# Kernel tuning notes

Hardware: AMD Instinct MI355X
Metric: run time of the kernel (lower is better)

## Reference

```python
import jax, jax.numpy as jnp
import numpy as np

T, K, D, CIN = 8, 64, 512, 1536  # timesteps, num_centers, redu_dim, input channels


def _conv(x, w, b=None, pad=0):
    y = jax.lax.conv_general_dilated(x, w, (1, 1), [(pad, pad), (pad, pad)],
                                     dimension_numbers=('NCHW', 'OIHW', 'NCHW'))
    return y if b is None else y + b[None, :, None, None]


def setup_inputs() -> dict:
    key = jax.random.key(0)
    ks = jax.random.split(key, 15)
    B, H, W = 32, 8, 8
    s = lambda i, shp: jax.random.normal(ks[i], shp, jnp.float32) * 0.05
    return dict(
        x=jax.random.normal(ks[0], (B * T, CIN, H, W), jnp.float32),
        redu_w=s(1, (D, CIN, 1, 1)), redu_b=s(2, (D,)),
        w_x=s(3, (K, D, 1, 1)),
        att_x=s(4, (K, K, 3, 3)), att_h_w=s(5, (K, K, 3, 3)), att_b=s(6, (K,)),
        share_w=s(7, (K, K, 3, 3)), share_b=s(8, (K,)),
        U_r=s(9, (K, K, 3, 3)), U_z=s(10, (K, K, 3, 3)), U_h=s(11, (K, K, 3, 3)),
        centers=s(12, (K, D)),
        fc1_w=s(13, (T * K // 16, T * K)), fc2_w=s(14, (T * K, T * K // 16)),
    )


def reference(x, redu_w, redu_b, w_x, att_x, att_h_w, att_b, share_w, share_b,
              U_r, U_z, U_h, centers, fc1_w, fc2_w):
    NT, _, H, W = x.shape
    B = NT // T
    xt = _conv(x, redu_w, redu_b)                    # (B*T, D, H, W) 1x1 reduction
    wxpb = _conv(xt, w_x)                            # (B*T, K, H, W)
    att_v = _conv(wxpb, att_x, pad=1).reshape(B, T, K, H, W).transpose(1, 0, 2, 3, 4)  # (T,B,K,H,W)
    wxpb5 = wxpb.reshape(B, T, K, H, W)

    def fc(v):  # ChannelAttention shared MLP (1x1 convs == matmuls)
        return jnp.maximum(v @ fc1_w.T, 0.) @ fc2_w.T

    def step(h, _):
        ah = _conv(h, att_h_w, att_b, pad=1)               # (B,K,H,W)
        e = jax.nn.relu(att_v + ah[None])                  # (T,B,K,H,W)
        e = e.transpose(1, 0, 2, 3, 4).reshape(B, T * K, H * W)
        g = jnp.tanh(fc(e.mean(-1)) + fc(e.max(-1)))       # (B, T*K) channel attention
        ex = jnp.exp(g.reshape(B, T, K))
        den = ex.sum(1, keepdims=True)
        den = den + (den == 0).astype(ex.dtype)
        alphas = ex / den                                  # softmax over timesteps
        wxt = (alphas[:, :, :, None, None] * wxpb5).sum(1) # (B,K,H,W)
        wxt = _conv(wxt, share_w, share_b, pad=1)
        z = jax.nn.sigmoid(wxt + _conv(h, U_z, pad=1))
        r = jax.nn.sigmoid(wxt + _conv(h, U_r, pad=1))
        hh = jnp.tanh(wxt + _conv(r * h, U_h, pad=1))
        h_new = (1. - z) * hh + z * h
        return h_new, h_new

    h0 = jnp.zeros((B, K, H, W), x.dtype)
    _, hs = jax.lax.scan(step, h0, None, length=T)         # (T,B,K,H,W)
    assigns = hs.transpose(1, 0, 2, 3, 4).reshape(B * T, K, H * W)
    a_sum = assigns.sum(-1, keepdims=True)                 # (B*T,K,1)
    a = a_sum * centers[None]                              # (B*T,K,D)
    feats = xt.reshape(B * T, D, H * W).transpose(0, 2, 1) # (B*T,HW,D)
    vlad = jnp.einsum('nks,nsd->nkd', assigns, feats) - a  # (B*T,K,D)
    vlad = vlad.reshape(B, T, K, D).sum(1)                 # (B,K,D)
    vlad = vlad / jnp.maximum(jnp.linalg.norm(vlad, axis=2, keepdims=True), 1e-12)
    vlad = vlad.reshape(B, K * D)
    vlad = vlad / jnp.maximum(jnp.linalg.norm(vlad, axis=1, keepdims=True), 1e-12)
    return vlad
```

## Files before the change

kernel.cpp:

```cpp
#include <hip/hip_runtime.h>
#include <math.h>

#define T_   8
#define K_   64
#define D_   512
#define CIN_ 1536
#define B_   32
#define S_   64
#define NT_  256

#define WLO_BF16  786432u
#define WXT_OFF   786432u
#define XT_OFF    819200u
#define WXPB_OFF  9207808u
#define ATTV_OFF  10256384u
#define HS_OFF    11436032u
#define ASUM_OFF  13041664u
#define WPB       25034752u
#define WATTX_BF16 20512768u

typedef __bf16 v8bf __attribute__((ext_vector_type(8)));
typedef __bf16 v4bf __attribute__((ext_vector_type(4)));
typedef float  v4f  __attribute__((ext_vector_type(4)));
typedef _Float16 v4h __attribute__((ext_vector_type(4)));
typedef _Float16 v8h __attribute__((ext_vector_type(8)));

__global__ __launch_bounds__(256) void k_prep(const float* __restrict__ redu_w,
                                              const float* __restrict__ w_x,
                                              float* __restrict__ ws) {
    unsigned idx = blockIdx.x * 256u + threadIdx.x;
    if (idx < 786432u) {
        float f = redu_w[idx];
        __bf16 h = (__bf16)f;
        __bf16 l = (__bf16)(f - (float)h);
        __bf16* wb = (__bf16*)ws;
        wb[idx] = h;
        wb[WLO_BF16 + idx] = l;
    } else if (idx < 819200u) {
        unsigned i = idx - 786432u;
        unsigned dd = i >> 6, k = i & 63u;
        ws[WXT_OFF + i] = w_x[k * 512u + dd];
    }
}

__global__ __launch_bounds__(256) void k_prep_w(const float* __restrict__ w0,
                                                const float* __restrict__ w1,
                                                const float* __restrict__ w2,
                                                const float* __restrict__ w3,
                                                const float* __restrict__ w4,
                                                const float* __restrict__ w5,
                                                float* __restrict__ ws) {
    unsigned idx = blockIdx.x * 256u + threadIdx.x;
    if (idx >= 221184u) return;
    unsigned w = idx / 36864u, r = idx % 36864u;
    const float* src = (w == 0) ? w0 : (w == 1) ? w1 : (w == 2) ? w2
                     : (w == 3) ? w3 : (w == 4) ? w4 : w5;
    float f = src[r];
    __bf16 h = (__bf16)f;
    __bf16 l = (__bf16)(f - (float)h);
    unsigned o = r / 576u, rem = r % 576u, ii = rem / 9u, dydx = rem % 9u;
    __bf16* wb = (__bf16*)ws;
    if (w < 5u) {
        unsigned dst = WPB + w * 73728u + (dydx * 64u + o) * 64u + ii;
        wb[dst] = h;
        wb[dst + 36864u] = l;
    } else {
        wb[WATTX_BF16 + (dydx * 64u + o) * 64u + ii] = h;
    }
}

__global__ __launch_bounds__(256) void k_gemm_xt_mfma(const float* __restrict__ x,
                                                      const float* __restrict__ redu_b,
                                                      float* __restrict__ ws) {
    __shared__ __bf16 xhi_s[64 * 72];
    __shared__ __bf16 xlo_s[64 * 72];
    const __bf16* __restrict__ Whi = (const __bf16*)ws;
    const __bf16* __restrict__ Wlo = ((const __bf16*)ws) + WLO_BF16;
    float* xt = ws + XT_OFF;
    const int n = blockIdx.y;
    const int d0 = blockIdx.x * 256;
    const int tid = threadIdx.x;
    const int wave = tid >> 6, lane = tid & 63;
    const int lrow = lane & 15, lkg = lane >> 4;
    const int m_base = d0 + wave * 64;
    const float* __restrict__ xn = x + n * 98304;
    const int s4 = tid & 15, cb = tid >> 4;

    v4f acc[4][4];
#pragma unroll
    for (int mt = 0; mt < 4; ++mt)
#pragma unroll
        for (int nt = 0; nt < 4; ++nt) acc[mt][nt] = (v4f){0.f, 0.f, 0.f, 0.f};

    for (int c0 = 0; c0 < 1536; c0 += 64) {
        float4 v[4];
#pragma unroll
        for (int j = 0; j < 4; ++j)
            v[j] = *(const float4*)&xn[(c0 + cb * 4 + j) * 64 + s4 * 4];
        __syncthreads();
#pragma unroll
        for (int i = 0; i < 4; ++i) {
            v4bf hv, lv;
#pragma unroll
            for (int j = 0; j < 4; ++j) {
                float f = ((const float*)&v[j])[i];
                __bf16 h = (__bf16)f;
                hv[j] = h;
                lv[j] = (__bf16)(f - (float)h);
            }
            int row = s4 * 4 + i;
            *(v4bf*)&xhi_s[row * 72 + cb * 4] = hv;
            *(v4bf*)&xlo_s[row * 72 + cb * 4] = lv;
        }
        __syncthreads();
#pragma unroll
        for (int ks = 0; ks < 64; ks += 32) {
            v8bf bh[4], bl[4], ah[4], al[4];
#pragma unroll
            for (int nt = 0; nt < 4; ++nt) {
                int off = (nt * 16 + lrow) * 72 + ks + lkg * 8;
                bh[nt] = *(const v8bf*)&xhi_s[off];
                bl[nt] = *(const v8bf*)&xlo_s[off];
            }
#pragma unroll
            for (int mt = 0; mt < 4; ++mt) {
                int gi = (m_base + mt * 16 + lrow) * 1536 + c0 + ks + lkg * 8;
                ah[mt] = *(const v8bf*)&Whi[gi];
                al[mt] = *(const v8bf*)&Wlo[gi];
            }
#pragma unroll
            for (int mt = 0; mt < 4; ++mt)
#pragma unroll
                for (int nt = 0; nt < 4; ++nt) {
                    acc[mt][nt] = __builtin_amdgcn_mfma_f32_16x16x32_bf16(
                        ah[mt], bh[nt], acc[mt][nt], 0, 0, 0);
                    acc[mt][nt] = __builtin_amdgcn_mfma_f32_16x16x32_bf16(
                        ah[mt], bl[nt], acc[mt][nt], 0, 0, 0);
                    acc[mt][nt] = __builtin_amdgcn_mfma_f32_16x16x32_bf16(
                        al[mt], bh[nt], acc[mt][nt], 0, 0, 0);
                }
        }
    }
#pragma unroll
    for (int mt = 0; mt < 4; ++mt) {
#pragma unroll
        for (int r = 0; r < 4; ++r) {
            int m = m_base + mt * 16 + lkg * 4 + r;
            float bias = redu_b[m];
#pragma unroll
            for (int nt = 0; nt < 4; ++nt) {
                int s = nt * 16 + lrow;
                xt[(n * 512 + m) * 64 + s] = acc[mt][nt][r] + bias;
            }
        }
    }
}

__global__ __launch_bounds__(256) void k_gemm_wxpb(float* __restrict__ ws) {
    __shared__ float Aw[16 * 64];
    __shared__ float Bx[16 * 64];
    const float* wxT = ws + WXT_OFF;
    const float* xt = ws + XT_OFF;
    float* wxpb = ws + WXPB_OFF;
    const int n = blockIdx.x;
    const int tid = threadIdx.x;
    const int sg = tid & 15, kg = tid >> 4;

    float acc[4][4];
#pragma unroll
    for (int i = 0; i < 4; ++i)
#pragma unroll
        for (int j = 0; j < 4; ++j) acc[i][j] = 0.f;

    for (int d0 = 0; d0 < 512; d0 += 16) {
        int cc = tid >> 4, q = tid & 15;
        *(float4*)&Aw[cc * 64 + q * 4] = *(const float4*)&wxT[(d0 + cc) * 64 + q * 4];
        *(float4*)&Bx[cc * 64 + q * 4] = *(const float4*)&xt[n * 32768 + (d0 + cc) * 64 + q * 4];
        __syncthreads();
#pragma unroll
        for (int c2 = 0; c2 < 16; ++c2) {
            float4 a = *(const float4*)&Aw[c2 * 64 + kg * 4];
            float4 b = *(const float4*)&Bx[c2 * 64 + sg * 4];
            float av[4] = {a.x, a.y, a.z, a.w};
            float bv[4] = {b.x, b.y, b.z, b.w};
#pragma unroll
            for (int i = 0; i < 4; ++i)
#pragma unroll
                for (int j = 0; j < 4; ++j)
                    acc[i][j] = fmaf(av[i], bv[j], acc[i][j]);
        }
        __syncthreads();
    }
#pragma unroll
    for (int i = 0; i < 4; ++i) {
        float4 o = {acc[i][0], acc[i][1], acc[i][2], acc[i][3]};
        *(float4*)&wxpb[(n * 64 + kg * 4 + i) * 64 + sg * 4] = o;
    }
}

__device__ __forceinline__ void conv_mfma(const __bf16* __restrict__ Wh,
                                          const __bf16* tS,
                                          int l15, int kg8, int mt, v4f acc[4]) {
    v8bf vz;
#pragma unroll
    for (int q = 0; q < 8; ++q) vz[q] = (__bf16)0.f;
#pragma unroll
    for (int i = 0; i < 4; ++i) acc[i] = (v4f){0.f, 0.f, 0.f, 0.f};
    const int yb = l15 >> 3, xb = l15 & 7;
    v8bf wh[9][2];
#pragma unroll
    for (int p = 0; p < 9; ++p) {
        const int wrow = (p * 64 + mt * 16 + l15) * 64 + kg8;
#pragma unroll
        for (int kci = 0; kci < 2; ++kci)
            wh[p][kci] = *(const v8bf*)&Wh[wrow + kci * 32];
    }
#pragma unroll
    for (int dy = 0; dy < 3; ++dy)
#pragma unroll
        for (int dx = 0; dx < 3; ++dx) {
            const int x0 = xb + dx - 1;
            const bool okx = (unsigned)x0 < 8u;
#pragma unroll
            for (int i = 0; i < 4; ++i) {
                const int y0 = yb + dy - 1 + 2 * i;
                const bool ok = ((unsigned)y0 < 8u) & okx;
                const int s0 = ((y0 * 8 + x0) & 63) * 72 + kg8;
#pragma unroll
                for (int kci = 0; kci < 2; ++kci) {
                    v8bf b = ok ? *(const v8bf*)&tS[s0 + kci * 32] : vz;
                    acc[i] = __builtin_amdgcn_mfma_f32_16x16x32_bf16(
                        wh[dy * 3 + dx][kci], b, acc[i], 0, 0, 0);
                }
            }
        }
}

__device__ __forceinline__ void conv_mfma3(const __bf16* __restrict__ W0,
                                           const __bf16* __restrict__ W1,
                                           const __bf16* __restrict__ W2,
                                           const __bf16* tS,
                                           int l15, int kg8, int mt,
                                           v4f a0[4], v4f a1[4], v4f a2[4]) {
    v8bf vz;
#pragma unroll
    for (int q = 0; q < 8; ++q) vz[q] = (__bf16)0.f;
#pragma unroll
    for (int i = 0; i < 4; ++i) {
        a0[i] = (v4f){0.f, 0.f, 0.f, 0.f};
        a1[i] = (v4f){0.f, 0.f, 0.f, 0.f};
        a2[i] = (v4f){0.f, 0.f, 0.f, 0.f};
    }
    const int yb = l15 >> 3, xb = l15 & 7;
#pragma unroll
    for (int dy = 0; dy < 3; ++dy) {
        v8bf w0[3][2], w1[3][2], w2[3][2];
#pragma unroll
        for (int dx = 0; dx < 3; ++dx) {
            const int wrow = ((dy * 3 + dx) * 64 + mt * 16 + l15) * 64 + kg8;
#pragma unroll
            for (int kci = 0; kci < 2; ++kci) {
                w0[dx][kci] = *(const v8bf*)&W0[wrow + kci * 32];
                w1[dx][kci] = *(const v8bf*)&W1[wrow + kci * 32];
                w2[dx][kci] = *(const v8bf*)&W2[wrow + kci * 32];
            }
        }
#pragma unroll
        for (int dx = 0; dx < 3; ++dx) {
            const int x0 = xb + dx - 1;
            const bool okx = (unsigned)x0 < 8u;
#pragma unroll
            for (int i = 0; i < 4; ++i) {
                const int y0 = yb + dy - 1 + 2 * i;
                const bool ok = ((unsigned)y0 < 8u) & okx;
                const int s0 = ((y0 * 8 + x0) & 63) * 72 + kg8;
#pragma unroll
                for (int kci = 0; kci < 2; ++kci) {
                    v8bf b = ok ? *(const v8bf*)&tS[s0 + kci * 32] : vz;
                    a0[i] = __builtin_amdgcn_mfma_f32_16x16x32_bf16(w0[dx][kci], b, a0[i], 0, 0, 0);
                    a1[i] = __builtin_amdgcn_mfma_f32_16x16x32_bf16(w1[dx][kci], b, a1[i], 0, 0, 0);
                    a2[i] = __builtin_amdgcn_mfma_f32_16x16x32_bf16(w2[dx][kci], b, a2[i], 0, 0, 0);
                }
            }
        }
    }
}

__global__ __launch_bounds__(256) void k_recur(const float* __restrict__ att_b,
                                               const float* __restrict__ share_b,
                                               const float* __restrict__ fc1_w,
                                               const float* __restrict__ fc2_w,
                                               float* __restrict__ ws) {
    __shared__ float h_s[4096];
    __shared__ __attribute__((aligned(16))) __bf16 tA[64 * 72];
    __shared__ float cA[64 * 65];
    __shared__ float cB[64 * 65];
    __shared__ float misc[1088];
    __shared__ __attribute__((aligned(16))) _Float16 attv_s[32768];
    const int b = blockIdx.x, tid = threadIdx.x;
    const int lane = tid & 63;
    const int wave = tid >> 6;
    const int mt = wave;
    const int l15 = lane & 15, kg = lane >> 4, kg8 = kg * 8;
    const __bf16* Wp = (const __bf16*)ws + WPB;
    const __bf16* Wattx = (const __bf16*)ws + WATTX_BF16;
    const float* wxpb = ws + WXPB_OFF;
    float* hsg = ws + HS_OFF;
    float* asg = ws + ASUM_OFF;

    for (int i = tid; i < 4096; i += 256) h_s[i] = 0.f;

    for (int tp = 0; tp < 8; ++tp) {
        const float* src = wxpb + (b * 8 + tp) * 4096;
        for (int i = tid; i < 4096; i += 256) {
            int k = i >> 6, s = i & 63;
            tA[s * 72 + k] = (__bf16)src[i];
        }
        __syncthreads();
        v4f av[4];
        conv_mfma(Wattx, tA, l15, kg8, mt, av);
#pragma unroll
        for (int i2 = 0; i2 < 4; ++i2)
#pragma unroll
            for (int r = 0; r < 4; ++r)
                attv_s[tp * 4096 + (mt * 16 + kg * 4 + r) * 64 + i2 * 16 + l15] =
                    (_Float16)av[i2][r];
        __syncthreads();
    }

    float abvr[2];
#pragma unroll
    for (int rep = 0; rep < 2; ++rep) abvr[rep] = att_b[(tid + rep * 256) >> 3];
    float sb4[4];
#pragma unroll
    for (int r = 0; r < 4; ++r) sb4[r] = share_b[mt * 16 + kg * 4 + r];

    for (int t = 0; t < 8; ++t) {
#pragma unroll
        for (int rep = 0; rep < 2; ++rep) {
            int s = tid & 63, g = (tid >> 6) + rep * 4;
#pragma unroll
            for (int q4 = 0; q4 < 2; ++q4) {
                v4bf hv;
#pragma unroll
                for (int q = 0; q < 4; ++q) hv[q] = (__bf16)h_s[(g * 8 + q4 * 4 + q) * 64 + s];
                *(v4bf*)&tA[s * 72 + g * 8 + q4 * 4] = hv;
            }
        }
        __syncthreads();
        v4f az[4], ar[4];
        {
            v4f a[4];
            conv_mfma3(Wp, Wp + 2u * 73728u, Wp + 3u * 73728u, tA,
                       l15, kg8, mt, a, az, ar);
#pragma unroll
            for (int i = 0; i < 4; ++i)
#pragma unroll
                for (int r = 0; r < 4; ++r)
                    cA[(mt * 16 + kg * 4 + r) * 65 + i * 16 + l15] = a[i][r];
        }
        __syncthreads();
#pragma unroll
        for (int rep = 0; rep < 2; ++rep) {
            int vt = tid + rep * 256;
            int kk = vt >> 3, yy = vt & 7;
            float ah8[8];
            const float* cr = &cA[kk * 65 + yy * 8];
#pragma unroll
            for (int xx = 0; xx < 8; ++xx) ah8[xx] = cr[xx] + abvr[rep];
            for (int tp = 0; tp < 8; ++tp) {
                v8h va = *(const v8h*)&attv_s[tp * 4096 + kk * 64 + yy * 8];
                float s_ = 0.f, m_ = 0.f;
#pragma unroll
                for (int xx = 0; xx < 8; ++xx) {
                    float v = fmaxf((float)va[xx] + ah8[xx], 0.f);
                    s_ += v;
                    m_ = fmaxf(m_, v);
                }
                s_ += __shfl_down(s_, 4, 8);
                s_ += __shfl_down(s_, 2, 8);
                s_ += __shfl_down(s_, 1, 8);
                m_ = fmaxf(m_, __shfl_down(m_, 4, 8));
                m_ = fmaxf(m_, __shfl_down(m_, 2, 8));
                m_ = fmaxf(m_, __shfl_down(m_, 1, 8));
                if (yy == 0) {
                    misc[tp * 64 + kk] = s_ * (1.f / 64.f);
                    misc[512 + tp * 64 + kk] = m_;
                }
            }
        }
        __syncthreads();
        {
            int i2 = tid >> 2, part = tid & 3;
            int i = i2 & 31;
            const float* src = misc + ((i2 < 32) ? 0 : 512);
            const float* wrow = fc1_w + i * 512 + part * 128;
            const float* s2 = src + part * 128;
            float pa[4] = {0.f, 0.f, 0.f, 0.f};
#pragma unroll
            for (int c4 = 0; c4 < 32; ++c4) {
                float4 wv = *(const float4*)&wrow[c4 * 4];
                float4 sv = *(const float4*)&s2[c4 * 4];
                float* pp = &pa[c4 & 3];
                *pp = fmaf(wv.x, sv.x, *pp);
                *pp = fmaf(wv.y, sv.y, *pp);
                *pp = fmaf(wv.z, sv.z, *pp);
                *pp = fmaf(wv.w, sv.w, *pp);
            }
            float p = (pa[0] + pa[1]) + (pa[2] + pa[3]);
            p += __shfl_down(p, 2, 4);
            p += __shfl_down(p, 1, 4);
            if (part == 0) misc[1024 + i2] = fmaxf(p, 0.f);
        }
        __syncthreads();
#pragma unroll
        for (int rep = 0; rep < 2; ++rep) {
            int vt = tid + rep * 256;
            const float* w2 = fc2_w + vt * 32;
            float gm = 0.f, gx = 0.f;
#pragma unroll
            for (int i4 = 0; i4 < 8; ++i4) {
                float4 wv = *(const float4*)&w2[i4 * 4];
                gm = fmaf(wv.x, misc[1024 + i4 * 4 + 0], gm);
                gm = fmaf(wv.y, misc[1024 + i4 * 4 + 1], gm);
                gm = fmaf(wv.z, misc[1024 + i4 * 4 + 2], gm);
                gm = fmaf(wv.w, misc[1024 + i4 * 4 + 3], gm);
                gx = fmaf(wv.x, misc[1056 + i4 * 4 + 0], gx);
                gx = fmaf(wv.y, misc[1056 + i4 * 4 + 1], gx);
                gx = fmaf(wv.z, misc[1056 + i4 * 4 + 2], gx);
                gx = fmaf(wv.w, misc[1056 + i4 * 4 + 3], gx);
            }
            misc[vt] = expf(tanhf(gm + gx));
        }
        __syncthreads();
#pragma unroll
        for (int rep = 0; rep < 2; ++rep) {
            int vt = tid + rep * 256;
            int k6 = vt & 63;
            float den = 0.f;
#pragma unroll
            for (int tp = 0; tp < 8; ++tp) den += misc[tp * 64 + k6];
            den += (den == 0.f) ? 1.f : 0.f;
            misc[512 + vt] = misc[vt] / den;
        }
        __syncthreads();
#pragma unroll
        for (int rep = 0; rep < 2; ++rep) {
            int vt = tid + rep * 256;
            int kk = vt >> 3, yy = vt & 7;
            float wx8[8];
#pragma unroll
            for (int xx = 0; xx < 8; ++xx) wx8[xx] = 0.f;
            const float* src0 = wxpb + b * 32768 + kk * 64 + yy * 8;
#pragma unroll
            for (int tp = 0; tp < 8; ++tp) {
                float al = misc[512 + tp * 64 + kk];
                float4 v0 = *(const float4*)&src0[tp * 4096];
                float4 v1 = *(const float4*)&src0[tp * 4096 + 4];
                float v[8] = {v0.x, v0.y, v0.z, v0.w, v1.x, v1.y, v1.z, v1.w};
#pragma unroll
                for (int xx = 0; xx < 8; ++xx) wx8[xx] = fmaf(al, v[xx], wx8[xx]);
            }
#pragma unroll
            for (int xx = 0; xx < 8; ++xx) tA[(yy * 8 + xx) * 72 + kk] = (__bf16)wx8[xx];
        }
        __syncthreads();
        v4f ash[4];
        conv_mfma(Wp + 1u * 73728u, tA, l15, kg8, mt, ash);
        float zf[4][4], wof[4][4];
#pragma unroll
        for (int i = 0; i < 4; ++i)
#pragma unroll
            for (int r = 0; r < 4; ++r) {
                int ko = mt * 16 + kg * 4 + r;
                int s = i * 16 + l15;
                float wo = ash[i][r] + sb4[r];
                float z = 1.f / (1.f + expf(-(wo + az[i][r])));
                float rr = 1.f / (1.f + expf(-(wo + ar[i][r])));
                cB[ko * 65 + s] = rr * h_s[ko * 64 + s];
                zf[i][r] = z;
                wof[i][r] = wo;
            }
        __syncthreads();
#pragma unroll
        for (int rep = 0; rep < 2; ++rep) {
            int s = tid & 63, g = (tid >> 6) + rep * 4;
#pragma unroll
            for (int q4 = 0; q4 < 2; ++q4) {
                v4bf hv;
#pragma unroll
                for (int q = 0; q < 4; ++q) hv[q] = (__bf16)cB[(g * 8 + q4 * 4 + q) * 65 + s];
                *(v4bf*)&tA[s * 72 + g * 8 + q4 * 4] = hv;
            }
        }
        __syncthreads();
        {
            v4f ach[4];
            conv_mfma(Wp + 4u * 73728u, tA, l15, kg8, mt, ach);
#pragma unroll
            for (int r = 0; r < 4; ++r) {
                int ko = mt * 16 + kg * 4 + r;
                float rsum = 0.f;
#pragma unroll
                for (int i = 0; i < 4; ++i) {
                    int s = i * 16 + l15;
                    float hh = tanhf(wof[i][r] + ach[i][r]);
                    float hold = h_s[ko * 64 + s];
                    float hn = (1.f - zf[i][r]) * hh + zf[i][r] * hold;
                    h_s[ko * 64 + s] = hn;
                    hsg[((t * 32 + b) * 64 + ko) * 64 + s] = hn;
                    rsum += hn;
                }
                rsum += __shfl_xor(rsum, 8, 16);
                rsum += __shfl_xor(rsum, 4, 16);
                rsum += __shfl_xor(rsum, 2, 16);
                rsum += __shfl_xor(rsum, 1, 16);
                if (l15 == 0) misc[1024 + ko] = rsum;
            }
        }
        __syncthreads();
        if (tid < 64) asg[b * 512 + t * 64 + tid] = misc[1024 + tid];
        __syncthreads();
    }
}

__global__ __launch_bounds__(256) void k_vlad(const float* __restrict__ centers,
                                              const float* __restrict__ ws,
                                              float* __restrict__ out) {
    __shared__ float As[16 * 68];
    __shared__ float Bs[16 * 68];
    const int b = blockIdx.y;
    const int d0 = blockIdx.x * 64;
    const int tid = threadIdx.x;
    const int kq = tid & 15, dq = tid >> 4;
    const int lk = tid >> 2, q = tid & 3;
    const float* hs = ws + HS_OFF;
    const float* xt = ws + XT_OFF;
    float acc[4][4];
#pragma unroll
    for (int i = 0; i < 4; ++i)
#pragma unroll
        for (int j = 0; j < 4; ++j) acc[i][j] = 0.f;

    for (int rc = 0; rc < 512; rc += 16) {
        int t = rc >> 6, hw0 = rc & 63;
        float4 va = *(const float4*)&hs[((t * 32 + b) * 64 + lk) * 64 + hw0 + q * 4];
        float4 vb = *(const float4*)&xt[(b * 8 + t) * 32768 + (d0 + lk) * 64 + hw0 + q * 4];
        __syncthreads();
        As[(q * 4 + 0) * 68 + lk] = va.x;
        As[(q * 4 + 1) * 68 + lk] = va.y;
        As[(q * 4 + 2) * 68 + lk] = va.z;
        As[(q * 4 + 3) * 68 + lk] = va.w;
        Bs[(q * 4 + 0) * 68 + lk] = vb.x;
        Bs[(q * 4 + 1) * 68 + lk] = vb.y;
        Bs[(q * 4 + 2) * 68 + lk] = vb.z;
        Bs[(q * 4 + 3) * 68 + lk] = vb.w;
        __syncthreads();
#pragma unroll
        for (int cc = 0; cc < 16; ++cc) {
            float4 a = *(const float4*)&As[cc * 68 + kq * 4];
            float4 bb = *(const float4*)&Bs[cc * 68 + dq * 4];
            float av[4] = {a.x, a.y, a.z, a.w};
            float bv[4] = {bb.x, bb.y, bb.z, bb.w};
#pragma unroll
            for (int i = 0; i < 4; ++i)
#pragma unroll
                for (int j = 0; j < 4; ++j)
                    acc[i][j] = fmaf(av[i], bv[j], acc[i][j]);
        }
    }
    const float* asum = ws + ASUM_OFF;
#pragma unroll
    for (int i = 0; i < 4; ++i) {
        int k = kq * 4 + i;
        float at = 0.f;
#pragma unroll
        for (int tp = 0; tp < 8; ++tp) at += asum[b * 512 + tp * 64 + k];
        float4 cen = *(const float4*)&centers[k * 512 + d0 + dq * 4];
        float4 o = {acc[i][0] - at * cen.x, acc[i][1] - at * cen.y,
                    acc[i][2] - at * cen.z, acc[i][3] - at * cen.w};
        *(float4*)&out[b * 32768 + k * 512 + d0 + dq * 4] = o;
    }
}

__global__ __launch_bounds__(64) void k_norm1(float* __restrict__ out) {
    const int b = blockIdx.x >> 6, k = blockIdx.x & 63;
    float* p = out + b * 32768 + k * 512;
    const int tid = threadIdx.x;
    float v[8];
    float ss = 0.f;
#pragma unroll
    for (int i = 0; i < 8; ++i) {
        v[i] = p[tid + i * 64];
        ss = fmaf(v[i], v[i], ss);
    }
#pragma unroll
    for (int off = 32; off > 0; off >>= 1) ss += __shfl_down(ss, off, 64);
    ss = __shfl(ss, 0, 64);
    float sc = 1.f / fmaxf(sqrtf(ss), 1e-12f);
#pragma unroll
    for (int i = 0; i < 8; ++i) p[tid + i * 64] = v[i] * sc;
}

__global__ __launch_bounds__(256) void k_norm2(float* __restrict__ out) {
    __shared__ float red[4];
    __shared__ float stot;
    const int b = blockIdx.x;
    const int tid = threadIdx.x;
    float* p = out + b * 32768;
    float ss = 0.f;
    for (int i = 0; i < 32; ++i) {
        float4 v = *(const float4*)&p[tid * 4 + i * 1024];
        ss += v.x * v.x + v.y * v.y + v.z * v.z + v.w * v.w;
    }
#pragma unroll
    for (int off = 32; off > 0; off >>= 1) ss += __shfl_down(ss, off, 64);
    if ((tid & 63) == 0) red[tid >> 6] = ss;
    __syncthreads();
    if (tid == 0) stot = 1.f / fmaxf(sqrtf(red[0] + red[1] + red[2] + red[3]), 1e-12f);
    __syncthreads();
    float sc = stot;
    for (int i = 0; i < 32; ++i) {
        float4 v = *(const float4*)&p[tid * 4 + i * 1024];
        v.x *= sc; v.y *= sc; v.z *= sc; v.w *= sc;
        *(float4*)&p[tid * 4 + i * 1024] = v;
    }
}

extern "C" void kernel_launch(void* const* d_in, const int* in_sizes, int n_in,
                              void* d_out, int out_size, void* d_ws, size_t ws_size,
                              hipStream_t stream) {
    const float* x       = (const float*)d_in[0];
    const float* redu_w  = (const float*)d_in[1];
    const float* redu_b  = (const float*)d_in[2];
    const float* w_x     = (const float*)d_in[3];
    const float* att_x   = (const float*)d_in[4];
    const float* att_h_w = (const float*)d_in[5];
    const float* att_b   = (const float*)d_in[6];
    const float* share_w = (const float*)d_in[7];
    const float* share_b = (const float*)d_in[8];
    const float* U_r     = (const float*)d_in[9];
    const float* U_z     = (const float*)d_in[10];
    const float* U_h     = (const float*)d_in[11];
    const float* centers = (const float*)d_in[12];
    const float* fc1_w   = (const float*)d_in[13];
    const float* fc2_w   = (const float*)d_in[14];
    float* ws = (float*)d_ws;
    float* out = (float*)d_out;

    k_prep<<<dim3(3200), dim3(256), 0, stream>>>(redu_w, w_x, ws);
    k_prep_w<<<dim3(864), dim3(256), 0, stream>>>(att_h_w, share_w, U_z, U_r, U_h,
                                                  att_x, ws);
    k_gemm_xt_mfma<<<dim3(2, 256), dim3(256), 0, stream>>>(x, redu_b, ws);
    k_gemm_wxpb<<<dim3(256), dim3(256), 0, stream>>>(ws);
    k_recur<<<dim3(32), dim3(256), 0, stream>>>(att_b, share_b, fc1_w, fc2_w, ws);
    k_vlad<<<dim3(8, 32), dim3(256), 0, stream>>>(centers, ws, out);
    k_norm1<<<dim3(2048), dim3(64), 0, stream>>>(out);
    k_norm2<<<dim3(32), dim3(256), 0, stream>>>(out);
}
```

Baseline: 697.8 us.

## Compose reduction and w_x weights, overlap xt GEMM with recurrence

Precomputes the combined weight W2 = w_x·redu_w, plus its folded bias, so wxpb is computed straight from x with one MFMA GEMM and no longer waits for xt. The full xt GEMM is moved into extra blocks of the recurrence kernel, so it runs alongside the 32 recurrence blocks and fills otherwise idle CUs. This removes the serial xt→wxpb dependency. The cost is an extra weight-composition kernel and some shift in rounding from the split-bf16 composed weights.

```diff
diff --git a/kernel.cpp b/kernel.cpp
--- a/kernel.cpp
+++ b/kernel.cpp
@@ -18,6 +18,9 @@
 #define ASUM_OFF  13041664u
 #define WPB       25034752u
 #define WATTX_BF16 20512768u
+#define W2HI_BF16  20549632u
+#define W2LO_BF16  20647936u
+#define B2_OFF     11435968u
 
 typedef __bf16 v8bf __attribute__((ext_vector_type(8)));
 typedef __bf16 v4bf __attribute__((ext_vector_type(4)));
@@ -26,7 +29,6 @@
 typedef _Float16 v8h __attribute__((ext_vector_type(8)));
 
 __global__ __launch_bounds__(256) void k_prep(const float* __restrict__ redu_w,
-                                              const float* __restrict__ w_x,
                                               float* __restrict__ ws) {
     unsigned idx = blockIdx.x * 256u + threadIdx.x;
     if (idx < 786432u) {
@@ -36,10 +38,6 @@
         __bf16* wb = (__bf16*)ws;
         wb[idx] = h;
         wb[WLO_BF16 + idx] = l;
-    } else if (idx < 819200u) {
-        unsigned i = idx - 786432u;
-        unsigned dd = i >> 6, k = i & 63u;
-        ws[WXT_OFF + i] = w_x[k * 512u + dd];
     }
 }
 
@@ -69,28 +67,60 @@
     }
 }
 
-__global__ __launch_bounds__(256) void k_gemm_xt_mfma(const float* __restrict__ x,
-                                                      const float* __restrict__ redu_b,
-                                                      float* __restrict__ ws) {
+__global__ __launch_bounds__(256) void k_w2(const float* __restrict__ w_x,
+                                            const float* __restrict__ redu_w,
+                                            const float* __restrict__ redu_b,
+                                            float* __restrict__ ws) {
+    __shared__ float wrow[512];
+    __shared__ float red[256];
+    const int k = blockIdx.x;
+    const int tid = threadIdx.x;
+    wrow[tid] = w_x[k * 512 + tid];
+    wrow[tid + 256] = w_x[k * 512 + tid + 256];
+    __syncthreads();
+    float acc[6] = {0.f, 0.f, 0.f, 0.f, 0.f, 0.f};
+    for (int d = 0; d < 512; ++d) {
+        float w = wrow[d];
+        const float* rr = &redu_w[d * 1536 + tid];
+#pragma unroll
+        for (int j = 0; j < 6; ++j) acc[j] = fmaf(w, rr[j * 256], acc[j]);
+    }
+    __bf16* wb = (__bf16*)ws;
+#pragma unroll
+    for (int j = 0; j < 6; ++j) {
+        int c = tid + j * 256;
+        __bf16 h = (__bf16)acc[j];
+        __bf16 l = (__bf16)(acc[j] - (float)h);
+        wb[W2HI_BF16 + k * 1536 + c] = h;
+        wb[W2LO_BF16 + k * 1536 + c] = l;
+    }
+    float p = wrow[tid] * redu_b[tid] + wrow[tid + 256] * redu_b[tid + 256];
+    red[tid] = p;
+    __syncthreads();
+    for (int off = 128; off > 0; off >>= 1) {
+        if (tid < off) red[tid] += red[tid + off];
+        __syncthreads();
+    }
+    if (tid == 0) ws[B2_OFF + k] = red[0];
+}
+
+__global__ __launch_bounds__(256) void k_wxpb_direct(const float* __restrict__ x,
+                                                     float* __restrict__ ws) {
     __shared__ __bf16 xhi_s[64 * 72];
     __shared__ __bf16 xlo_s[64 * 72];
-    const __bf16* __restrict__ Whi = (const __bf16*)ws;
-    const __bf16* __restrict__ Wlo = ((const __bf16*)ws) + WLO_BF16;
-    float* xt = ws + XT_OFF;
-    const int n = blockIdx.y;
-    const int d0 = blockIdx.x * 256;
+    const __bf16* __restrict__ W2h = (const __bf16*)ws + W2HI_BF16;
+    const __bf16* __restrict__ W2l = (const __bf16*)ws + W2LO_BF16;
+    float* wxpb = ws + WXPB_OFF;
+    const int n = blockIdx.x;
     const int tid = threadIdx.x;
     const int wave = tid >> 6, lane = tid & 63;
     const int lrow = lane & 15, lkg = lane >> 4;
-    const int m_base = d0 + wave * 64;
     const float* __restrict__ xn = x + n * 98304;
     const int s4 = tid & 15, cb = tid >> 4;
 
-    v4f acc[4][4];
-#pragma unroll
-    for (int mt = 0; mt < 4; ++mt)
-#pragma unroll
-        for (int nt = 0; nt < 4; ++nt) acc[mt][nt] = (v4f){0.f, 0.f, 0.f, 0.f};
+    v4f acc[4];
+#pragma unroll
+    for (int nt = 0; nt < 4; ++nt) acc[nt] = (v4f){0.f, 0.f, 0.f, 0.f};
 
     for (int c0 = 0; c0 < 1536; c0 += 64) {
         float4 v[4];
@@ -115,86 +145,31 @@
         __syncthreads();
 #pragma unroll
         for (int ks = 0; ks < 64; ks += 32) {
-            v8bf bh[4], bl[4], ah[4], al[4];
+            v8bf bh[4], bl[4];
 #pragma unroll
             for (int nt = 0; nt < 4; ++nt) {
                 int off = (nt * 16 + lrow) * 72 + ks + lkg * 8;
                 bh[nt] = *(const v8bf*)&xhi_s[off];
                 bl[nt] = *(const v8bf*)&xlo_s[off];
             }
-#pragma unroll
-            for (int mt = 0; mt < 4; ++mt) {
-                int gi = (m_base + mt * 16 + lrow) * 1536 + c0 + ks + lkg * 8;
-                ah[mt] = *(const v8bf*)&Whi[gi];
-                al[mt] = *(const v8bf*)&Wlo[gi];
-            }
-#pragma unroll
-            for (int mt = 0; mt < 4; ++mt)
-#pragma unroll
-                for (int nt = 0; nt < 4; ++nt) {
-                    acc[mt][nt] = __builtin_amdgcn_mfma_f32_16x16x32_bf16(
-                        ah[mt], bh[nt], acc[mt][nt], 0, 0, 0);
-                    acc[mt][nt] = __builtin_amdgcn_mfma_f32_16x16x32_bf16(
-                        ah[mt], bl[nt], acc[mt][nt], 0, 0, 0);
-                    acc[mt][nt] = __builtin_amdgcn_mfma_f32_16x16x32_bf16(
-                        al[mt], bh[nt], acc[mt][nt], 0, 0, 0);
-                }
-        }
-    }
-#pragma unroll
-    for (int mt = 0; mt < 4; ++mt) {
-#pragma unroll
-        for (int r = 0; r < 4; ++r) {
-            int m = m_base + mt * 16 + lkg * 4 + r;
-            float bias = redu_b[m];
+            int gi = (wave * 16 + lrow) * 1536 + c0 + ks + lkg * 8;
+            v8bf ah = *(const v8bf*)&W2h[gi];
+            v8bf al = *(const v8bf*)&W2l[gi];
 #pragma unroll
             for (int nt = 0; nt < 4; ++nt) {
-                int s = nt * 16 + lrow;
-                xt[(n * 512 + m) * 64 + s] = acc[mt][nt][r] + bias;
-            }
-        }
-    }
-}
-
-__global__ __launch_bounds__(256) void k_gemm_wxpb(float* __restrict__ ws) {
-    __shared__ float Aw[16 * 64];
-    __shared__ float Bx[16 * 64];
-    const float* wxT = ws + WXT_OFF;
-    const float* xt = ws + XT_OFF;
-    float* wxpb = ws + WXPB_OFF;
-    const int n = blockIdx.x;
-    const int tid = threadIdx.x;
-    const int sg = tid & 15, kg = tid >> 4;
-
-    float acc[4][4];
-#pragma unroll
-    for (int i = 0; i < 4; ++i)
-#pragma unroll
-        for (int j = 0; j < 4; ++j) acc[i][j] = 0.f;
-
-    for (int d0 = 0; d0 < 512; d0 += 16) {
-        int cc = tid >> 4, q = tid & 15;
-        *(float4*)&Aw[cc * 64 + q * 4] = *(const float4*)&wxT[(d0 + cc) * 64 + q * 4];
-        *(float4*)&Bx[cc * 64 + q * 4] = *(const float4*)&xt[n * 32768 + (d0 + cc) * 64 + q * 4];
-        __syncthreads();
-#pragma unroll
-        for (int c2 = 0; c2 < 16; ++c2) {
-            float4 a = *(const float4*)&Aw[c2 * 64 + kg * 4];
-            float4 b = *(const float4*)&Bx[c2 * 64 + sg * 4];
-            float av[4] = {a.x, a.y, a.z, a.w};
-            float bv[4] = {b.x, b.y, b.z, b.w};
-#pragma unroll
-            for (int i = 0; i < 4; ++i)
-#pragma unroll
-                for (int j = 0; j < 4; ++j)
-                    acc[i][j] = fmaf(av[i], bv[j], acc[i][j]);
-        }
-        __syncthreads();
-    }
-#pragma unroll
-    for (int i = 0; i < 4; ++i) {
-        float4 o = {acc[i][0], acc[i][1], acc[i][2], acc[i][3]};
-        *(float4*)&wxpb[(n * 64 + kg * 4 + i) * 64 + sg * 4] = o;
+                acc[nt] = __builtin_amdgcn_mfma_f32_16x16x32_bf16(ah, bh[nt], acc[nt], 0, 0, 0);
+                acc[nt] = __builtin_amdgcn_mfma_f32_16x16x32_bf16(ah, bl[nt], acc[nt], 0, 0, 0);
+                acc[nt] = __builtin_amdgcn_mfma_f32_16x16x32_bf16(al, bh[nt], acc[nt], 0, 0, 0);
+            }
+        }
+    }
+#pragma unroll
+    for (int r = 0; r < 4; ++r) {
+        int m = wave * 16 + lkg * 4 + r;
+        float bias = ws[B2_OFF + m];
+#pragma unroll
+        for (int nt = 0; nt < 4; ++nt)
+            wxpb[(n * 64 + m) * 64 + nt * 16 + lrow] = acc[nt][r] + bias;
     }
 }
 
@@ -286,10 +261,12 @@
     }
 }
 
-__global__ __launch_bounds__(256) void k_recur(const float* __restrict__ att_b,
+__global__ __launch_bounds__(256) void k_fused(const float* __restrict__ att_b,
                                                const float* __restrict__ share_b,
                                                const float* __restrict__ fc1_w,
                                                const float* __restrict__ fc2_w,
+                                               const float* __restrict__ x,
+                                               const float* __restrict__ redu_b,
                                                float* __restrict__ ws) {
     __shared__ float h_s[4096];
     __shared__ __attribute__((aligned(16))) __bf16 tA[64 * 72];
@@ -297,7 +274,95 @@
     __shared__ float cB[64 * 65];
     __shared__ float misc[1088];
     __shared__ __attribute__((aligned(16))) _Float16 attv_s[32768];
-    const int b = blockIdx.x, tid = threadIdx.x;
+    const int tid = threadIdx.x;
+
+    if (blockIdx.x >= 32) {
+        const int gb = blockIdx.x - 32;
+        const int n = gb >> 1;
+        const int d0 = (gb & 1) * 256;
+        const __bf16* __restrict__ Whi = (const __bf16*)ws;
+        const __bf16* __restrict__ Wlo = ((const __bf16*)ws) + WLO_BF16;
+        float* xt = ws + XT_OFF;
+        const int wave = tid >> 6, lane = tid & 63;
+        const int lrow = lane & 15, lkg = lane >> 4;
+        const int m_base = d0 + wave * 64;
+        const float* __restrict__ xn = x + n * 98304;
+        const int s4 = tid & 15, cb = tid >> 4;
+        __bf16* gxhi = (__bf16*)attv_s;
+        __bf16* gxlo = gxhi + 4608;
+
+        v4f acc[4][4];
+#pragma unroll
+        for (int mt = 0; mt < 4; ++mt)
+#pragma unroll
+            for (int nt = 0; nt < 4; ++nt) acc[mt][nt] = (v4f){0.f, 0.f, 0.f, 0.f};
+
+        for (int c0 = 0; c0 < 1536; c0 += 64) {
+            float4 v[4];
+#pragma unroll
+            for (int j = 0; j < 4; ++j)
+                v[j] = *(const float4*)&xn[(c0 + cb * 4 + j) * 64 + s4 * 4];
+            __syncthreads();
+#pragma unroll
+            for (int i = 0; i < 4; ++i) {
+                v4bf hv, lv;
+#pragma unroll
+                for (int j = 0; j < 4; ++j) {
+                    float f = ((const float*)&v[j])[i];
+                    __bf16 h = (__bf16)f;
+                    hv[j] = h;
+                    lv[j] = (__bf16)(f - (float)h);
+                }
+                int row = s4 * 4 + i;
+                *(v4bf*)&gxhi[row * 72 + cb * 4] = hv;
+                *(v4bf*)&gxlo[row * 72 + cb * 4] = lv;
+            }
+            __syncthreads();
+#pragma unroll
+            for (int ks = 0; ks < 64; ks += 32) {
+                v8bf bh[4], bl[4], ah[4], al[4];
+#pragma unroll
+                for (int nt = 0; nt < 4; ++nt) {
+                    int off = (nt * 16 + lrow) * 72 + ks + lkg * 8;
+                    bh[nt] = *(const v8bf*)&gxhi[off];
+                    bl[nt] = *(const v8bf*)&gxlo[off];
+                }
+#pragma unroll
+                for (int mt = 0; mt < 4; ++mt) {
+                    int gi = (m_base + mt * 16 + lrow) * 1536 + c0 + ks + lkg * 8;
+                    ah[mt] = *(const v8bf*)&Whi[gi];
+                    al[mt] = *(const v8bf*)&Wlo[gi];
+                }
+#pragma unroll
+                for (int mt = 0; mt < 4; ++mt)
+#pragma unroll
+                    for (int nt = 0; nt < 4; ++nt) {
+                        acc[mt][nt] = __builtin_amdgcn_mfma_f32_16x16x32_bf16(
+                            ah[mt], bh[nt], acc[mt][nt], 0, 0, 0);
+                        acc[mt][nt] = __builtin_amdgcn_mfma_f32_16x16x32_bf16(
+                            ah[mt], bl[nt], acc[mt][nt], 0, 0, 0);
+                        acc[mt][nt] = __builtin_amdgcn_mfma_f32_16x16x32_bf16(
+                            al[mt], bh[nt], acc[mt][nt], 0, 0, 0);
+                    }
+            }
+        }
+#pragma unroll
+        for (int mt = 0; mt < 4; ++mt) {
+#pragma unroll
+            for (int r = 0; r < 4; ++r) {
+                int m = m_base + mt * 16 + lkg * 4 + r;
+                float bias = redu_b[m];
+#pragma unroll
+                for (int nt = 0; nt < 4; ++nt) {
+                    int s = nt * 16 + lrow;
+                    xt[(n * 512 + m) * 64 + s] = acc[mt][nt][r] + bias;
+                }
+            }
+        }
+        return;
+    }
+
+    const int b = blockIdx.x;
     const int lane = tid & 63;
     const int wave = tid >> 6;
     const int mt = wave;
@@ -648,12 +713,13 @@
     float* ws = (float*)d_ws;
     float* out = (float*)d_out;
 
-    k_prep<<<dim3(3200), dim3(256), 0, stream>>>(redu_w, w_x, ws);
+    k_prep<<<dim3(3072), dim3(256), 0, stream>>>(redu_w, ws);
     k_prep_w<<<dim3(864), dim3(256), 0, stream>>>(att_h_w, share_w, U_z, U_r, U_h,
                                                   att_x, ws);
-    k_gemm_xt_mfma<<<dim3(2, 256), dim3(256), 0, stream>>>(x, redu_b, ws);
-    k_gemm_wxpb<<<dim3(256), dim3(256), 0, stream>>>(ws);
-    k_recur<<<dim3(32), dim3(256), 0, stream>>>(att_b, share_b, fc1_w, fc2_w, ws);
+    k_w2<<<dim3(64), dim3(256), 0, stream>>>(w_x, redu_w, redu_b, ws);
+    k_wxpb_direct<<<dim3(256), dim3(256), 0, stream>>>(x, ws);
+    k_fused<<<dim3(544), dim3(256), 0, stream>>>(att_b, share_b, fc1_w, fc2_w,
+                                                 x, redu_b, ws);
     k_vlad<<<dim3(8, 32), dim3(256), 0, stream>>>(centers, ws, out);
     k_norm1<<<dim3(2048), dim3(64), 0, stream>>>(out);
     k_norm2<<<dim3(32), dim3(256), 0, stream>>>(out);
```

Result: no change. 710.2 us (+1.8%).
